# Kernel tuning notes

Hardware: AMD Instinct MI355X
Metric: run time of the kernel (lower is better)

Reference implementation:

```python
import jax, jax.numpy as jnp
import numpy as np

EMB = 128
EA = 32
ET = 32
N = 50000
E = 500000
EPS = 1e-5
DROP_P = 0.1


def setup_inputs() -> dict:
    key = jax.random.key(0)
    ks = jax.random.split(key, 12)
    din = EMB + EA + ET
    return {
        "hidden": jax.random.normal(ks[0], (N, EMB), jnp.float32),
        "edge_index": jax.random.randint(ks[1], (2, E), 0, N, jnp.int64 if jax.config.jax_enable_x64 else jnp.int32),
        "edge_attr": jax.random.normal(ks[2], (E, EA), jnp.float32),
        "edge_time_emb": jax.random.normal(ks[3], (E, ET), jnp.float32),
        "boundary_condition": jax.random.normal(ks[4], (N, EMB), jnp.float32),
        # learned params (torch Linear stored transposed: [in, out])
        "W_msg": jax.random.normal(ks[5], (din, EMB), jnp.float32) / np.sqrt(din),
        "b_msg": jnp.zeros((EMB,), jnp.float32),
        "W_lin": jax.random.normal(ks[6], (EMB, EMB), jnp.float32) / np.sqrt(EMB),
        "b_lin": jnp.zeros((EMB,), jnp.float32),
        "ln_gamma": jnp.ones((EMB,), jnp.float32),
        "ln_beta": jnp.zeros((EMB,), jnp.float32),
    }


def reference(hidden, edge_index, edge_attr, edge_time_emb, boundary_condition,
              W_msg, b_msg, W_lin, b_lin, ln_gamma, ln_beta):
    num_nodes = hidden.shape[0]
    # gather source node features, concat with edge features -> [E, emb+ea+et]
    msg = jnp.concatenate([hidden[edge_index[0]], edge_attr, edge_time_emb], axis=1)
    msg = jax.nn.relu(msg @ W_msg + b_msg)                      # [E, emb]
    # append boundary condition as self-loop messages
    msg_aug = jnp.concatenate([msg, boundary_condition], axis=0)
    idx_aug = jnp.concatenate([edge_index[1], jnp.arange(num_nodes, dtype=edge_index.dtype)])
    out = jax.ops.segment_sum(msg_aug, idx_aug, num_segments=num_nodes)  # scatter-sum [N, emb]
    out = out @ W_lin + b_lin
    # LayerNorm (eps=1e-5, affine)
    mean = out.mean(-1, keepdims=True)
    var = out.var(-1, keepdims=True)
    out = (out - mean) * jax.lax.rsqrt(var + EPS) * ln_gamma + ln_beta
    out = jax.nn.relu(out)
    # dropout p=0.1, training=True (fixed key for reproducibility)
    keep = jax.random.bernoulli(jax.random.key(42), 1.0 - DROP_P, out.shape)
    out = jnp.where(keep, out / (1.0 - DROP_P), 0.0)
    return out
```

## Files before the change

kernel.cpp:

```cpp
#include <hip/hip_runtime.h>
#include <stdint.h>

#define NN 50000
#define NE 500000
#define NEPAD 500032
#define SPB 64
#define NT_BLOCKS ((NN + 63) / 64)
#define DEG_STRIDE (NT_BLOCKS * 256)
#define NBLK_N ((NN + 255) / 256)

typedef short bf16x8 __attribute__((ext_vector_type(8)));
typedef float f32x4 __attribute__((ext_vector_type(4)));
typedef unsigned short u16;
typedef unsigned short u16x4 __attribute__((ext_vector_type(4)));
typedef unsigned int u32x4 __attribute__((ext_vector_type(4)));

__device__ __forceinline__ u16 f2b(float x) {
  uint32_t u = __builtin_bit_cast(uint32_t, x);
  return (u16)((u + 0x7fffu + ((u >> 16) & 1u)) >> 16);
}
__device__ __forceinline__ float b2f(uint32_t lo16) {
  return __builtin_bit_cast(float, lo16 << 16);
}

__device__ __forceinline__ void threefry(uint32_t x0, uint32_t x1,
                                         uint32_t& o0, uint32_t& o1) {
  const uint32_t k0 = 0u, k1 = 42u, k2 = 0u ^ 42u ^ 0x1BD11BDAu;
  x0 += k0; x1 += k1;
#define TFR(r) { x0 += x1; x1 = (x1 << r) | (x1 >> (32 - r)); x1 ^= x0; }
  TFR(13) TFR(15) TFR(26) TFR(6)
  x0 += k1; x1 += k2 + 1u;
  TFR(17) TFR(29) TFR(16) TFR(24)
  x0 += k2; x1 += k0 + 2u;
  TFR(13) TFR(15) TFR(26) TFR(6)
  x0 += k0; x1 += k1 + 3u;
  TFR(17) TFR(29) TFR(16) TFR(24)
  x0 += k1; x1 += k2 + 4u;
  TFR(13) TFR(15) TFR(26) TFR(6)
  x0 += k2; x1 += k0 + 5u;
#undef TFR
  o0 = x0; o1 = x1;
}

__device__ __forceinline__ bool jax_keep(uint32_t j) {
  uint32_t o0, o1;
  threefry(0u, j, o0, o1);
  uint32_t bits = o0 ^ o1;
  float u = __builtin_bit_cast(float, (bits >> 9) | 0x3f800000u) - 1.0f;
  return u < 0.9f;
}

__global__ __launch_bounds__(256) void k_prep(const float* __restrict__ Wmsg,
                                              const float* __restrict__ Wlin,
                                              u16* __restrict__ WhImg,
                                              u16* __restrict__ WcImg,
                                              u16* __restrict__ WlImg) {
  const int t = threadIdx.x, b = blockIdx.x;
  if (b == 0) {
#pragma unroll
    for (int it = 0; it < 16; ++it) {
      int g = t + (it << 8);
      int d = g >> 5, k4 = (g & 31) << 2;
      u16x4 v = {f2b(Wmsg[(k4 + 0) * 128 + d]), f2b(Wmsg[(k4 + 1) * 128 + d]),
                 f2b(Wmsg[(k4 + 2) * 128 + d]), f2b(Wmsg[(k4 + 3) * 128 + d])};
      *(u16x4*)&WhImg[(d << 7) + k4] = v;
    }
  } else if (b == 1) {
#pragma unroll
    for (int it = 0; it < 8; ++it) {
      int g = t + (it << 8);
      int d = g >> 4, k4 = (g & 15) << 2;
      u16x4 v = {f2b(Wmsg[(128 + k4 + 0) * 128 + d]), f2b(Wmsg[(128 + k4 + 1) * 128 + d]),
                 f2b(Wmsg[(128 + k4 + 2) * 128 + d]), f2b(Wmsg[(128 + k4 + 3) * 128 + d])};
      *(u16x4*)&WcImg[(d << 6) + k4] = v;
    }
  } else {
#pragma unroll
    for (int it = 0; it < 16; ++it) {
      int g = t + (it << 8);
      int d = g >> 5, k4 = (g & 31) << 2;
      u16x4 v = {f2b(Wlin[(k4 + 0) * 128 + d]), f2b(Wlin[(k4 + 1) * 128 + d]),
                 f2b(Wlin[(k4 + 2) * 128 + d]), f2b(Wlin[(k4 + 3) * 128 + d])};
      *(u16x4*)&WlImg[(d << 7) + k4] = v;
    }
  }
}

__global__ __launch_bounds__(256) void k_scan1(const uint32_t* __restrict__ deg,
                                               uint32_t* __restrict__ ex,
                                               uint32_t* __restrict__ bsum) {
  __shared__ uint32_t s[256];
  int t = threadIdx.x;
  int i = blockIdx.x * 256 + t;
  uint32_t v = (i < NN) ? deg[i] : 0u;
  s[t] = v;
  __syncthreads();
#pragma unroll
  for (int off = 1; off < 256; off <<= 1) {
    uint32_t y = (t >= off) ? s[t - off] : 0u;
    __syncthreads();
    s[t] += y;
    __syncthreads();
  }
  if (i < NN) ex[i] = s[t] - v;
  if (t == 255) bsum[blockIdx.x] = s[255];
}

__global__ __launch_bounds__(256) void k_scan2(const uint32_t* __restrict__ bsum,
                                               uint32_t* __restrict__ boff) {
  __shared__ uint32_t s[256];
  int t = threadIdx.x;
  uint32_t v = (t < NBLK_N) ? bsum[t] : 0u;
  s[t] = v;
  __syncthreads();
#pragma unroll
  for (int off = 1; off < 256; off <<= 1) {
    uint32_t y = (t >= off) ? s[t - off] : 0u;
    __syncthreads();
    s[t] += y;
    __syncthreads();
  }
  boff[t] = s[t] - v;
}

__global__ __launch_bounds__(256) void k_scan3(const uint32_t* __restrict__ ex,
                                               const uint32_t* __restrict__ boff,
                                               uint32_t* __restrict__ cursor) {
  int i = blockIdx.x * 256 + threadIdx.x;
  if (i < NN) cursor[i] = ex[i] + boff[blockIdx.x];
}

__global__ __launch_bounds__(256) void k_perm_s(const int* __restrict__ ei,
                                                const float* __restrict__ attr,
                                                const float* __restrict__ tim,
                                                uint32_t* __restrict__ cursor,
                                                u16* __restrict__ Asorted,
                                                uint32_t* __restrict__ sd) {
  const int t = threadIdx.x;
  const int j = t & 7;
  const long e = (long)blockIdx.x * 32 + (t >> 3);
  const bool v = e < NE;
  uint32_t pos = 0, sdv = 0;
  if (v && j == 0) {
    uint32_t src = (uint32_t)ei[e];
    uint32_t dst = (uint32_t)ei[NE + e];
    sdv = src | (dst << 16);
    pos = atomicAdd(&cursor[dst], 1u);
  }
  pos = __shfl(pos, 0, 8);
  if (v) {
    f32x4 va = *(const f32x4*)(attr + ((size_t)e << 5) + (j << 2));
    f32x4 vt = *(const f32x4*)(tim + ((size_t)e << 5) + (j << 2));
    u16x4 ba = {f2b(va[0]), f2b(va[1]), f2b(va[2]), f2b(va[3])};
    u16x4 bt = {f2b(vt[0]), f2b(vt[1]), f2b(vt[2]), f2b(vt[3])};
    *(u16x4*)&Asorted[((size_t)pos << 6) + (j << 2)] = ba;
    *(u16x4*)&Asorted[((size_t)pos << 6) + 32 + (j << 2)] = bt;
    if (j == 0) sd[pos] = sdv;
  }
}

__global__ __launch_bounds__(256) void k_perm_f(const int* __restrict__ ei,
                                                uint32_t* __restrict__ cursor,
                                                int* __restrict__ perm,
                                                uint32_t* __restrict__ sd) {
  int i = blockIdx.x * 256 + threadIdx.x;
  if (i < NE) {
    uint32_t s = (uint32_t)ei[i], d = (uint32_t)ei[NE + i];
    uint32_t pos = atomicAdd(&cursor[d], 1u);
    perm[pos] = i;
    sd[pos] = s | (d << 16);
  }
}

__global__ __launch_bounds__(256) void k_hp(const float* __restrict__ hidden,
                                            const u16* __restrict__ WhImg,
                                            const float* __restrict__ bmsg,
                                            const int* __restrict__ ei,
                                            uint32_t* __restrict__ deg,
                                            u16* __restrict__ Hp) {
  __shared__ u16 sA[64 * 128];
  const int t = threadIdx.x;
  const int row0 = blockIdx.x << 6;
  for (int i = blockIdx.x * 256 + t; i < NE; i += DEG_STRIDE)
    atomicAdd(&deg[ei[NE + i]], 1u);
#pragma unroll
  for (int it = 0; it < 8; ++it) {
    int li = t + (it << 8);
    int row = li >> 5, c4 = li & 31;
    int n = row0 + row;
    f32x4 v = {0.f, 0.f, 0.f, 0.f};
    if (n < NN) v = *(const f32x4*)(hidden + ((size_t)n << 7) + (c4 << 2));
    u16x4 b = {f2b(v[0]), f2b(v[1]), f2b(v[2]), f2b(v[3])};
    *(u16x4*)&sA[(row << 7) + ((((c4 >> 1) ^ (row & 15)) << 3) + ((c4 & 1) << 2))] = b;
  }
  __syncthreads();
  const int lane = t & 63, w = t >> 6;
  const int quad = lane >> 4, lr = lane & 15;
  f32x4 c[4][2];
#pragma unroll
  for (int i = 0; i < 4; ++i)
#pragma unroll
    for (int j = 0; j < 2; ++j) { f32x4 z = {0.f, 0.f, 0.f, 0.f}; c[i][j] = z; }
#pragma unroll
  for (int ks = 0; ks < 128; ks += 32) {
    const int gi = (ks >> 3) + quad;
    bf16x8 a[4], b[2];
#pragma unroll
    for (int i = 0; i < 4; ++i) {
      int row = (i << 4) + lr;
      a[i] = *(const bf16x8*)&sA[(row << 7) + ((gi ^ (row & 15)) << 3)];
    }
#pragma unroll
    for (int j = 0; j < 2; ++j) {
      int col = (w << 5) + (j << 4) + lr;
      b[j] = *(const bf16x8*)&WhImg[(col << 7) + (gi << 3)];
    }
#pragma unroll
    for (int i = 0; i < 4; ++i)
#pragma unroll
      for (int j = 0; j < 2; ++j)
        c[i][j] = __builtin_amdgcn_mfma_f32_16x16x32_bf16(a[i], b[j], c[i][j], 0, 0, 0);
  }
#pragma unroll
  for (int j = 0; j < 2; ++j) {
    int d = (w << 5) + (j << 4) + lr;
    float bias = bmsg[d];
#pragma unroll
    for (int i = 0; i < 4; ++i) {
      int nb = row0 + (i << 4) + (quad << 2);
#pragma unroll
      for (int r = 0; r < 4; ++r) {
        int n = nb + r;
        if (n < NN) Hp[((size_t)n << 7) + d] = f2b(c[i][j][r] + bias);
      }
    }
  }
}

template <bool SORTED>
__global__ __launch_bounds__(256, 4) void k_edge3(const float* __restrict__ attr,
                                                  const float* __restrict__ tim,
                                                  const int* __restrict__ perm,
                                                  const u16* __restrict__ Asorted,
                                                  const u16* __restrict__ WcImg,
                                                  const uint32_t* __restrict__ sd,
                                                  const u16* __restrict__ Hp,
                                                  float* __restrict__ acc) {
  __shared__ union { u16 A[64 * 64]; float C[64 * 128]; } lds;
  __shared__ int sdst[64];
  const int t = threadIdx.x;
  const long e0 = (long)blockIdx.x << 6;

  if (!SORTED) {
#pragma unroll
    for (int it = 0; it < 2; ++it) {
      int li = t + (it << 8);
      int row = li >> 3, c4 = li & 7;
      long sg = e0 + row;
      f32x4 va = {0.f, 0.f, 0.f, 0.f}, vt = {0.f, 0.f, 0.f, 0.f};
      if (sg < NE) {
        int e = perm[sg];
        va = *(const f32x4*)(attr + ((size_t)e << 5) + (c4 << 2));
        vt = *(const f32x4*)(tim + ((size_t)e << 5) + (c4 << 2));
      }
      int g0 = c4 >> 1, h = (c4 & 1) << 2;
      u16x4 ba = {f2b(va[0]), f2b(va[1]), f2b(va[2]), f2b(va[3])};
      u16x4 bt = {f2b(vt[0]), f2b(vt[1]), f2b(vt[2]), f2b(vt[3])};
      *(u16x4*)&lds.A[(row << 6) + (((g0 ^ (row & 7)) << 3) + h)] = ba;
      *(u16x4*)&lds.A[(row << 6) + ((((g0 + 4) ^ (row & 7)) << 3) + h)] = bt;
    }
  }
  const int s = t >> 2, q = t & 3;
  const long sg1 = e0 + s;
  const bool v1 = sg1 < NE;
  int src = 0, dstn = -1;
  if (v1) {
    uint32_t sdv = sd[sg1];
    src = (int)(sdv & 0xffffu);
    dstn = (int)(sdv >> 16);
  }
  u32x4 hp[4];
  if (v1) {
    const u32x4* hp4 = (const u32x4*)(Hp + ((size_t)src << 7) + (q << 5));
#pragma unroll
    for (int g = 0; g < 4; ++g) hp[g] = hp4[g];
  }
  if (q == 0) sdst[s] = v1 ? dstn : -1;
  __syncthreads();

  const int lane = t & 63, w = t >> 6;
  const int quad = lane >> 4, lr = lane & 15;
  f32x4 c[4][2];
#pragma unroll
  for (int i = 0; i < 4; ++i)
#pragma unroll
    for (int j = 0; j < 2; ++j) { f32x4 z = {0.f, 0.f, 0.f, 0.f}; c[i][j] = z; }
#pragma unroll
  for (int ks = 0; ks < 64; ks += 32) {
    const int gi = (ks >> 3) + quad;
    bf16x8 a[4], b[2];
#pragma unroll
    for (int i = 0; i < 4; ++i) {
      int row = (i << 4) + lr;
      if (SORTED)
        a[i] = *(const bf16x8*)&Asorted[((size_t)(e0 + row) << 6) + (gi << 3)];
      else
        a[i] = *(const bf16x8*)&lds.A[(row << 6) + ((gi ^ (row & 7)) << 3)];
    }
#pragma unroll
    for (int j = 0; j < 2; ++j) {
      int col = (w << 5) + (j << 4) + lr;
      b[j] = *(const bf16x8*)&WcImg[(col << 6) + (gi << 3)];
    }
#pragma unroll
    for (int i = 0; i < 4; ++i)
#pragma unroll
      for (int j = 0; j < 2; ++j)
        c[i][j] = __builtin_amdgcn_mfma_f32_16x16x32_bf16(a[i], b[j], c[i][j], 0, 0, 0);
  }
  __syncthreads();
#pragma unroll
  for (int i = 0; i < 4; ++i)
#pragma unroll
    for (int j = 0; j < 2; ++j)
#pragma unroll
      for (int r = 0; r < 4; ++r) {
        int row = (i << 4) + (quad << 2) + r;
        int col = (w << 5) + (j << 4) + lr;
        lds.C[(row << 7) + ((((col >> 2) ^ (row & 31)) << 2) + (col & 3))] = c[i][j][r];
      }
  __syncthreads();
  if (v1) {
#pragma unroll
    for (int g = 0; g < 8; ++g) {
      int cb = (q << 5) + (g << 2);
      float* p = &lds.C[(s << 7) + ((((cb >> 2) ^ (s & 31)) << 2))];
      f32x4 cv = *(const f32x4*)p;
      uint32_t w0 = hp[g >> 1][(g & 1) << 1];
      uint32_t w1 = hp[g >> 1][((g & 1) << 1) + 1];
      cv[0] = fmaxf(cv[0] + b2f(w0 & 0xffffu), 0.f);
      cv[1] = fmaxf(cv[1] + b2f(w0 >> 16), 0.f);
      cv[2] = fmaxf(cv[2] + b2f(w1 & 0xffffu), 0.f);
      cv[3] = fmaxf(cv[3] + b2f(w1 >> 16), 0.f);
      *(f32x4*)p = cv;
    }
  }
  __syncthreads();
  {
    const int col = t & 127, half = t >> 7;
    const int beg = half << 5, end = beg + 32;
    int cur = sdst[beg];
    float sum = 0.f;
    int runstart = beg;
    for (int ss = beg; ss < end; ++ss) {
      int d = sdst[ss];
      if (d != cur) {
        if (cur >= 0) {
          float* p = acc + ((size_t)cur << 7) + col;
          if (runstart == beg) unsafeAtomicAdd(p, sum);
          else *p = sum;
        }
        cur = d; sum = 0.f; runstart = ss;
      }
      sum += lds.C[(ss << 7) + ((((col >> 2) ^ (ss & 31)) << 2) + (col & 3))];
    }
    if (cur >= 0) unsafeAtomicAdd(acc + ((size_t)cur << 7) + col, sum);
  }
}

__global__ __launch_bounds__(256) void k_out(float* accout,
                                             const float* __restrict__ bnd,
                                             const u16* __restrict__ WlImg,
                                             const float* __restrict__ blin,
                                             const float* __restrict__ gam,
                                             const float* __restrict__ bet) {
  __shared__ union { u16 A[64 * 128]; float C[64 * 128]; } lds;
  const int t = threadIdx.x;
  const int row0 = blockIdx.x << 6;
#pragma unroll
  for (int it = 0; it < 8; ++it) {
    int li = t + (it << 8);
    int row = li >> 5, c4 = li & 31;
    int n = row0 + row;
    f32x4 v = {0.f, 0.f, 0.f, 0.f};
    if (n < NN) {
      f32x4 a = *(const f32x4*)(accout + ((size_t)n << 7) + (c4 << 2));
      f32x4 b = *(const f32x4*)(bnd + ((size_t)n << 7) + (c4 << 2));
      v = a + b;
    }
    u16x4 bb = {f2b(v[0]), f2b(v[1]), f2b(v[2]), f2b(v[3])};
    *(u16x4*)&lds.A[(row << 7) + ((((c4 >> 1) ^ (row & 15)) << 3) + ((c4 & 1) << 2))] = bb;
  }
  __syncthreads();
  const int lane = t & 63, w = t >> 6;
  const int quad = lane >> 4, lr = lane & 15;
  f32x4 c[4][2];
#pragma unroll
  for (int i = 0; i < 4; ++i)
#pragma unroll
    for (int j = 0; j < 2; ++j) { f32x4 z = {0.f, 0.f, 0.f, 0.f}; c[i][j] = z; }
#pragma unroll
  for (int ks = 0; ks < 128; ks += 32) {
    const int gi = (ks >> 3) + quad;
    bf16x8 a[4], b[2];
#pragma unroll
    for (int i = 0; i < 4; ++i) {
      int row = (i << 4) + lr;
      a[i] = *(const bf16x8*)&lds.A[(row << 7) + ((gi ^ (row & 15)) << 3)];
    }
#pragma unroll
    for (int j = 0; j < 2; ++j) {
      int col = (w << 5) + (j << 4) + lr;
      b[j] = *(const bf16x8*)&WlImg[(col << 7) + (gi << 3)];
    }
#pragma unroll
    for (int i = 0; i < 4; ++i)
#pragma unroll
      for (int j = 0; j < 2; ++j)
        c[i][j] = __builtin_amdgcn_mfma_f32_16x16x32_bf16(a[i], b[j], c[i][j], 0, 0, 0);
  }
  __syncthreads();
#pragma unroll
  for (int i = 0; i < 4; ++i)
#pragma unroll
    for (int j = 0; j < 2; ++j)
#pragma unroll
      for (int r = 0; r < 4; ++r) {
        int row = (i << 4) + (quad << 2) + r;
        int col = (w << 5) + (j << 4) + lr;
        lds.C[(row << 7) + ((((col >> 2) ^ (row & 31)) << 2) + (col & 3))] = c[i][j][r];
      }
  __syncthreads();
  const int row = t >> 2, q = t & 3;
  const int n = row0 + row;
  float s1 = 0.f, s2 = 0.f;
  if (n < NN) {
#pragma unroll
    for (int g = 0; g < 8; ++g) {
      int g5 = (q << 3) + g;
      f32x4 cv = *(const f32x4*)&lds.C[(row << 7) + ((g5 ^ (row & 31)) << 2)];
      f32x4 bl = *(const f32x4*)(blin + (g5 << 2));
#pragma unroll
      for (int m = 0; m < 4; ++m) {
        float x = cv[m] + bl[m];
        s1 += x; s2 += x * x;
      }
    }
  }
  s1 += __shfl_xor(s1, 1, 64); s1 += __shfl_xor(s1, 2, 64);
  s2 += __shfl_xor(s2, 1, 64); s2 += __shfl_xor(s2, 2, 64);
  if (n < NN) {
    const float mean = s1 * 0.0078125f;
    const float var = s2 * 0.0078125f - mean * mean;
    const float inv = 1.0f / sqrtf(var + 1e-5f);
#pragma unroll
    for (int g = 0; g < 8; ++g) {
      int g5 = (q << 3) + g;
      int d0 = g5 << 2;
      f32x4 cv = *(const f32x4*)&lds.C[(row << 7) + ((g5 ^ (row & 31)) << 2)];
      f32x4 bl = *(const f32x4*)(blin + d0);
      f32x4 gm = *(const f32x4*)(gam + d0);
      f32x4 bb = *(const f32x4*)(bet + d0);
      f32x4 o;
#pragma unroll
      for (int m = 0; m < 4; ++m) {
        float x = cv[m] + bl[m];
        float y = fmaxf((x - mean) * inv * gm[m] + bb[m], 0.f);
        uint32_t jj = ((uint32_t)n << 7) + (uint32_t)(d0 + m);
        o[m] = jax_keep(jj) ? (y * (1.0f / 0.9f)) : 0.0f;
      }
      *(f32x4*)(accout + ((size_t)n << 7) + d0) = o;
    }
  }
}

extern "C" void kernel_launch(void* const* d_in, const int* in_sizes, int n_in,
                              void* d_out, int out_size, void* d_ws, size_t ws_size,
                              hipStream_t stream) {
  (void)in_sizes; (void)n_in; (void)out_size;
  const float* hidden = (const float*)d_in[0];
  const int*   ei     = (const int*)d_in[1];
  const float* attr   = (const float*)d_in[2];
  const float* tim    = (const float*)d_in[3];
  const float* bnd    = (const float*)d_in[4];
  const float* Wmsg   = (const float*)d_in[5];
  const float* bmsg   = (const float*)d_in[6];
  const float* Wlin   = (const float*)d_in[7];
  const float* blin   = (const float*)d_in[8];
  const float* gam    = (const float*)d_in[9];
  const float* bet    = (const float*)d_in[10];

  float* acc = (float*)d_out;

  char* ws = (char*)d_ws;
  u16*      Hp     = (u16*)(ws + 0);
  u16*      WhImg  = (u16*)(ws + 12800000);
  u16*      WcImg  = (u16*)(ws + 12832768);
  u16*      WlImg  = (u16*)(ws + 12849152);
  uint32_t* deg    = (uint32_t*)(ws + 12881920);
  uint32_t* cursor = (uint32_t*)(ws + 13081920);
  uint32_t* bsum   = (uint32_t*)(ws + 13281920);
  uint32_t* boff   = (uint32_t*)(ws + 13282944);
  uint32_t* ex     = (uint32_t*)(ws + 13283968);
  uint32_t* sd     = (uint32_t*)(ws + 13483968);
  u16*      Asort  = (u16*)(ws + 15484096);
  int*      perm   = (int*)(ws + 15484096);
  const bool sorted = ws_size >= (size_t)(15484096 + (size_t)NEPAD * 64 * 2);

  hipMemsetAsync(deg, 0, (size_t)NN * 4, stream);
  hipMemsetAsync(acc, 0, (size_t)NN * 128 * 4, stream);

  k_prep <<<dim3(3), dim3(256), 0, stream>>>(Wmsg, Wlin, WhImg, WcImg, WlImg);
  k_hp   <<<dim3(NT_BLOCKS), dim3(256), 0, stream>>>(hidden, WhImg, bmsg, ei, deg, Hp);
  k_scan1<<<dim3(NBLK_N), dim3(256), 0, stream>>>(deg, ex, bsum);
  k_scan2<<<dim3(1), dim3(256), 0, stream>>>(bsum, boff);
  k_scan3<<<dim3(NBLK_N), dim3(256), 0, stream>>>(ex, boff, cursor);
  if (sorted) {
    k_perm_s<<<dim3((NE + 31) / 32), dim3(256), 0, stream>>>(ei, attr, tim, cursor, Asort, sd);
    k_edge3<true><<<dim3(NEPAD / SPB), dim3(256), 0, stream>>>(attr, tim, nullptr, Asort, WcImg, sd, Hp, acc);
  } else {
    k_perm_f<<<dim3((NE + 255) / 256), dim3(256), 0, stream>>>(ei, cursor, perm, sd);
    k_edge3<false><<<dim3(NEPAD / SPB), dim3(256), 0, stream>>>(attr, tim, perm, nullptr, WcImg, sd, Hp, acc);
  }
  k_out  <<<dim3(NT_BLOCKS), dim3(256), 0, stream>>>(acc, bnd, WlImg, blin, gam, bet);
}
```

Before: 372.3 us.

## Convert edge features to bf16 in original order and gather via perm

Replaces the sorted-scatter path, which wrote bf16 edge features into destination-sorted positions, with one that converts attr/time to bf16 in original edge order using coalesced writes and records only a permutation. The edge kernel then gathers 128-byte bf16 rows through perm into LDS and reads src/dst from edge_index through perm instead of a packed sd array. This removes the scattered writes and the sd buffer and always takes a single path. The cost is indirect gathers in the edge kernel, including an extra dependent perm->ei lookup.

```diff
diff --git a/kernel.cpp b/kernel.cpp
--- a/kernel.cpp
+++ b/kernel.cpp
@@ -13,6 +13,7 @@
 typedef float f32x4 __attribute__((ext_vector_type(4)));
 typedef unsigned short u16;
 typedef unsigned short u16x4 __attribute__((ext_vector_type(4)));
+typedef unsigned short u16x8 __attribute__((ext_vector_type(8)));
 typedef unsigned int u32x4 __attribute__((ext_vector_type(4)));
 
 __device__ __forceinline__ u16 f2b(float x) {
@@ -130,120 +131,34 @@
   if (i < NN) cursor[i] = ex[i] + boff[blockIdx.x];
 }
 
-__global__ __launch_bounds__(256) void k_perm_s(const int* __restrict__ ei,
-                                                const float* __restrict__ attr,
-                                                const float* __restrict__ tim,
-                                                uint32_t* __restrict__ cursor,
-                                                u16* __restrict__ Asorted,
-                                                uint32_t* __restrict__ sd) {
+__global__ __launch_bounds__(256) void k_permconv(const int* __restrict__ ei,
+                                                  const float* __restrict__ attr,
+                                                  const float* __restrict__ tim,
+                                                  uint32_t* __restrict__ cursor,
+                                                  u16* __restrict__ Abf,
+                                                  int* __restrict__ perm) {
   const int t = threadIdx.x;
   const int j = t & 7;
   const long e = (long)blockIdx.x * 32 + (t >> 3);
-  const bool v = e < NE;
-  uint32_t pos = 0, sdv = 0;
-  if (v && j == 0) {
-    uint32_t src = (uint32_t)ei[e];
+  if (e >= NE) return;
+  const float* src8 = (j < 4) ? (attr + ((size_t)e << 5) + (j << 3))
+                              : (tim + ((size_t)e << 5) + ((j - 4) << 3));
+  f32x4 v0 = *(const f32x4*)src8;
+  f32x4 v1 = *(const f32x4*)(src8 + 4);
+  u16x8 b = {f2b(v0[0]), f2b(v0[1]), f2b(v0[2]), f2b(v0[3]),
+             f2b(v1[0]), f2b(v1[1]), f2b(v1[2]), f2b(v1[3])};
+  *(u16x8*)&Abf[((size_t)e << 6) + (j << 3)] = b;
+  if (j == 0) {
     uint32_t dst = (uint32_t)ei[NE + e];
-    sdv = src | (dst << 16);
-    pos = atomicAdd(&cursor[dst], 1u);
-  }
-  pos = __shfl(pos, 0, 8);
-  if (v) {
-    f32x4 va = *(const f32x4*)(attr + ((size_t)e << 5) + (j << 2));
-    f32x4 vt = *(const f32x4*)(tim + ((size_t)e << 5) + (j << 2));
-    u16x4 ba = {f2b(va[0]), f2b(va[1]), f2b(va[2]), f2b(va[3])};
-    u16x4 bt = {f2b(vt[0]), f2b(vt[1]), f2b(vt[2]), f2b(vt[3])};
-    *(u16x4*)&Asorted[((size_t)pos << 6) + (j << 2)] = ba;
-    *(u16x4*)&Asorted[((size_t)pos << 6) + 32 + (j << 2)] = bt;
-    if (j == 0) sd[pos] = sdv;
-  }
-}
-
-__global__ __launch_bounds__(256) void k_perm_f(const int* __restrict__ ei,
-                                                uint32_t* __restrict__ cursor,
-                                                int* __restrict__ perm,
-                                                uint32_t* __restrict__ sd) {
-  int i = blockIdx.x * 256 + threadIdx.x;
-  if (i < NE) {
-    uint32_t s = (uint32_t)ei[i], d = (uint32_t)ei[NE + i];
-    uint32_t pos = atomicAdd(&cursor[d], 1u);
-    perm[pos] = i;
-    sd[pos] = s | (d << 16);
-  }
-}
-
-__global__ __launch_bounds__(256) void k_hp(const float* __restrict__ hidden,
-                                            const u16* __restrict__ WhImg,
-                                            const float* __restrict__ bmsg,
-                                            const int* __restrict__ ei,
-                                            uint32_t* __restrict__ deg,
-                                            u16* __restrict__ Hp) {
-  __shared__ u16 sA[64 * 128];
-  const int t = threadIdx.x;
-  const int row0 = blockIdx.x << 6;
-  for (int i = blockIdx.x * 256 + t; i < NE; i += DEG_STRIDE)
-    atomicAdd(&deg[ei[NE + i]], 1u);
-#pragma unroll
-  for (int it = 0; it < 8; ++it) {
-    int li = t + (it << 8);
-    int row = li >> 5, c4 = li & 31;
-    int n = row0 + row;
-    f32x4 v = {0.f, 0.f, 0.f, 0.f};
-    if (n < NN) v = *(const f32x4*)(hidden + ((size_t)n << 7) + (c4 << 2));
-    u16x4 b = {f2b(v[0]), f2b(v[1]), f2b(v[2]), f2b(v[3])};
-    *(u16x4*)&sA[(row << 7) + ((((c4 >> 1) ^ (row & 15)) << 3) + ((c4 & 1) << 2))] = b;
-  }
-  __syncthreads();
-  const int lane = t & 63, w = t >> 6;
-  const int quad = lane >> 4, lr = lane & 15;
-  f32x4 c[4][2];
-#pragma unroll
-  for (int i = 0; i < 4; ++i)
-#pragma unroll
-    for (int j = 0; j < 2; ++j) { f32x4 z = {0.f, 0.f, 0.f, 0.f}; c[i][j] = z; }
-#pragma unroll
-  for (int ks = 0; ks < 128; ks += 32) {
-    const int gi = (ks >> 3) + quad;
-    bf16x8 a[4], b[2];
-#pragma unroll
-    for (int i = 0; i < 4; ++i) {
-      int row = (i << 4) + lr;
-      a[i] = *(const bf16x8*)&sA[(row << 7) + ((gi ^ (row & 15)) << 3)];
-    }
-#pragma unroll
-    for (int j = 0; j < 2; ++j) {
-      int col = (w << 5) + (j << 4) + lr;
-      b[j] = *(const bf16x8*)&WhImg[(col << 7) + (gi << 3)];
-    }
-#pragma unroll
-    for (int i = 0; i < 4; ++i)
-#pragma unroll
-      for (int j = 0; j < 2; ++j)
-        c[i][j] = __builtin_amdgcn_mfma_f32_16x16x32_bf16(a[i], b[j], c[i][j], 0, 0, 0);
-  }
-#pragma unroll
-  for (int j = 0; j < 2; ++j) {
-    int d = (w << 5) + (j << 4) + lr;
-    float bias = bmsg[d];
-#pragma unroll
-    for (int i = 0; i < 4; ++i) {
-      int nb = row0 + (i << 4) + (quad << 2);
-#pragma unroll
-      for (int r = 0; r < 4; ++r) {
-        int n = nb + r;
-        if (n < NN) Hp[((size_t)n << 7) + d] = f2b(c[i][j][r] + bias);
-      }
-    }
-  }
-}
-
-template <bool SORTED>
-__global__ __launch_bounds__(256, 4) void k_edge3(const float* __restrict__ attr,
-                                                  const float* __restrict__ tim,
-                                                  const int* __restrict__ perm,
-                                                  const u16* __restrict__ Asorted,
+    uint32_t pos = atomicAdd(&cursor[dst], 1u);
+    perm[pos] = (int)e;
+  }
+}
+
+__global__ __launch_bounds__(256, 4) void k_edge3(const int* __restrict__ perm,
+                                                  const u16* __restrict__ Abf,
+                                                  const int* __restrict__ ei,
                                                   const u16* __restrict__ WcImg,
-                                                  const uint32_t* __restrict__ sd,
                                                   const u16* __restrict__ Hp,
                                                   float* __restrict__ acc) {
   __shared__ union { u16 A[64 * 64]; float C[64 * 128]; } lds;
@@ -251,33 +166,26 @@
   const int t = threadIdx.x;
   const long e0 = (long)blockIdx.x << 6;
 
-  if (!SORTED) {
-#pragma unroll
-    for (int it = 0; it < 2; ++it) {
-      int li = t + (it << 8);
-      int row = li >> 3, c4 = li & 7;
-      long sg = e0 + row;
-      f32x4 va = {0.f, 0.f, 0.f, 0.f}, vt = {0.f, 0.f, 0.f, 0.f};
-      if (sg < NE) {
-        int e = perm[sg];
-        va = *(const f32x4*)(attr + ((size_t)e << 5) + (c4 << 2));
-        vt = *(const f32x4*)(tim + ((size_t)e << 5) + (c4 << 2));
-      }
-      int g0 = c4 >> 1, h = (c4 & 1) << 2;
-      u16x4 ba = {f2b(va[0]), f2b(va[1]), f2b(va[2]), f2b(va[3])};
-      u16x4 bt = {f2b(vt[0]), f2b(vt[1]), f2b(vt[2]), f2b(vt[3])};
-      *(u16x4*)&lds.A[(row << 6) + (((g0 ^ (row & 7)) << 3) + h)] = ba;
-      *(u16x4*)&lds.A[(row << 6) + ((((g0 + 4) ^ (row & 7)) << 3) + h)] = bt;
-    }
+#pragma unroll
+  for (int it = 0; it < 2; ++it) {
+    int li = t + (it << 8);
+    int row = li >> 3, g = li & 7;
+    long sg = e0 + row;
+    u32x4 v = {0u, 0u, 0u, 0u};
+    if (sg < NE) {
+      int e = perm[sg];
+      v = *(const u32x4*)(Abf + ((size_t)e << 6) + (g << 3));
+    }
+    *(u32x4*)&lds.A[(row << 6) + ((g ^ (row & 7)) << 3)] = v;
   }
   const int s = t >> 2, q = t & 3;
   const long sg1 = e0 + s;
   const bool v1 = sg1 < NE;
   int src = 0, dstn = -1;
   if (v1) {
-    uint32_t sdv = sd[sg1];
-    src = (int)(sdv & 0xffffu);
-    dstn = (int)(sdv >> 16);
+    int e = perm[sg1];
+    src = ei[e];
+    dstn = ei[NE + e];
   }
   u32x4 hp[4];
   if (v1) {
@@ -302,10 +210,7 @@
 #pragma unroll
     for (int i = 0; i < 4; ++i) {
       int row = (i << 4) + lr;
-      if (SORTED)
-        a[i] = *(const bf16x8*)&Asorted[((size_t)(e0 + row) << 6) + (gi << 3)];
-      else
-        a[i] = *(const bf16x8*)&lds.A[(row << 6) + ((gi ^ (row & 7)) << 3)];
+      a[i] = *(const bf16x8*)&lds.A[(row << 6) + ((gi ^ (row & 7)) << 3)];
     }
 #pragma unroll
     for (int j = 0; j < 2; ++j) {
@@ -368,6 +273,71 @@
   }
 }
 
+__global__ __launch_bounds__(256) void k_hp(const float* __restrict__ hidden,
+                                            const u16* __restrict__ WhImg,
+                                            const float* __restrict__ bmsg,
+                                            const int* __restrict__ ei,
+                                            uint32_t* __restrict__ deg,
+                                            u16* __restrict__ Hp) {
+  __shared__ u16 sA[64 * 128];
+  const int t = threadIdx.x;
+  const int row0 = blockIdx.x << 6;
+  for (int i = blockIdx.x * 256 + t; i < NE; i += DEG_STRIDE)
+    atomicAdd(&deg[ei[NE + i]], 1u);
+#pragma unroll
+  for (int it = 0; it < 8; ++it) {
+    int li = t + (it << 8);
+    int row = li >> 5, c4 = li & 31;
+    int n = row0 + row;
+    f32x4 v = {0.f, 0.f, 0.f, 0.f};
+    if (n < NN) v = *(const f32x4*)(hidden + ((size_t)n << 7) + (c4 << 2));
+    u16x4 b = {f2b(v[0]), f2b(v[1]), f2b(v[2]), f2b(v[3])};
+    *(u16x4*)&sA[(row << 7) + ((((c4 >> 1) ^ (row & 15)) << 3) + ((c4 & 1) << 2))] = b;
+  }
+  __syncthreads();
+  const int lane = t & 63, w = t >> 6;
+  const int quad = lane >> 4, lr = lane & 15;
+  f32x4 c[4][2];
+#pragma unroll
+  for (int i = 0; i < 4; ++i)
+#pragma unroll
+    for (int j = 0; j < 2; ++j) { f32x4 z = {0.f, 0.f, 0.f, 0.f}; c[i][j] = z; }
+#pragma unroll
+  for (int ks = 0; ks < 128; ks += 32) {
+    const int gi = (ks >> 3) + quad;
+    bf16x8 a[4], b[2];
+#pragma unroll
+    for (int i = 0; i < 4; ++i) {
+      int row = (i << 4) + lr;
+      a[i] = *(const bf16x8*)&sA[(row << 7) + ((gi ^ (row & 15)) << 3)];
+    }
+#pragma unroll
+    for (int j = 0; j < 2; ++j) {
+      int col = (w << 5) + (j << 4) + lr;
+      b[j] = *(const bf16x8*)&WhImg[(col << 7) + (gi << 3)];
+    }
+#pragma unroll
+    for (int i = 0; i < 4; ++i)
+#pragma unroll
+      for (int j = 0; j < 2; ++j)
+        c[i][j] = __builtin_amdgcn_mfma_f32_16x16x32_bf16(a[i], b[j], c[i][j], 0, 0, 0);
+  }
+#pragma unroll
+  for (int j = 0; j < 2; ++j) {
+    int d = (w << 5) + (j << 4) + lr;
+    float bias = bmsg[d];
+#pragma unroll
+    for (int i = 0; i < 4; ++i) {
+      int nb = row0 + (i << 4) + (quad << 2);
+#pragma unroll
+      for (int r = 0; r < 4; ++r) {
+        int n = nb + r;
+        if (n < NN) Hp[((size_t)n << 7) + d] = f2b(c[i][j][r] + bias);
+      }
+    }
+  }
+}
+
 __global__ __launch_bounds__(256) void k_out(float* accout,
                                              const float* __restrict__ bnd,
                                              const u16* __restrict__ WlImg,
@@ -477,7 +447,7 @@
 extern "C" void kernel_launch(void* const* d_in, const int* in_sizes, int n_in,
                               void* d_out, int out_size, void* d_ws, size_t ws_size,
                               hipStream_t stream) {
-  (void)in_sizes; (void)n_in; (void)out_size;
+  (void)in_sizes; (void)n_in; (void)out_size; (void)ws_size;
   const float* hidden = (const float*)d_in[0];
   const int*   ei     = (const int*)d_in[1];
   const float* attr   = (const float*)d_in[2];
@@ -502,10 +472,8 @@
   uint32_t* bsum   = (uint32_t*)(ws + 13281920);
   uint32_t* boff   = (uint32_t*)(ws + 13282944);
   uint32_t* ex     = (uint32_t*)(ws + 13283968);
-  uint32_t* sd     = (uint32_t*)(ws + 13483968);
-  u16*      Asort  = (u16*)(ws + 15484096);
-  int*      perm   = (int*)(ws + 15484096);
-  const bool sorted = ws_size >= (size_t)(15484096 + (size_t)NEPAD * 64 * 2);
+  int*      perm   = (int*)(ws + 13483968);
+  u16*      Abf    = (u16*)(ws + 15484096);
 
   hipMemsetAsync(deg, 0, (size_t)NN * 4, stream);
   hipMemsetAsync(acc, 0, (size_t)NN * 128 * 4, stream);
@@ -515,12 +483,7 @@
   k_scan1<<<dim3(NBLK_N), dim3(256), 0, stream>>>(deg, ex, bsum);
   k_scan2<<<dim3(1), dim3(256), 0, stream>>>(bsum, boff);
   k_scan3<<<dim3(NBLK_N), dim3(256), 0, stream>>>(ex, boff, cursor);
-  if (sorted) {
-    k_perm_s<<<dim3((NE + 31) / 32), dim3(256), 0, stream>>>(ei, attr, tim, cursor, Asort, sd);
-    k_edge3<true><<<dim3(NEPAD / SPB), dim3(256), 0, stream>>>(attr, tim, nullptr, Asort, WcImg, sd, Hp, acc);
-  } else {
-    k_perm_f<<<dim3((NE + 255) / 256), dim3(256), 0, stream>>>(ei, cursor, perm, sd);
-    k_edge3<false><<<dim3(NEPAD / SPB), dim3(256), 0, stream>>>(attr, tim, perm, nullptr, WcImg, sd, Hp, acc);
-  }
+  k_permconv<<<dim3(NE / 32), dim3(256), 0, stream>>>(ei, attr, tim, cursor, Abf, perm);
+  k_edge3<<<dim3(NEPAD / SPB), dim3(256), 0, stream>>>(perm, Abf, ei, WcImg, Hp, acc);
   k_out  <<<dim3(NT_BLOCKS), dim3(256), 0, stream>>>(acc, bnd, WlImg, blin, gam, bet);
 }
```

Measured after the change: 373.3 us. No clear change (+0.3%).
